# Optimization experiments

Measured on AMD Instinct MI355X. Metric: run time of the kernel, lower is better.

The kernel has to match this reference:

```python
import jax, jax.numpy as jnp
import numpy as np

TEMPERATURE = 0.07
EPS = 1e-20

def setup_inputs() -> dict:
    key = jax.random.key(0)
    k1, k2 = jax.random.split(key)
    B, D, L = 4096, 256, 20
    features = jax.random.normal(k1, (B, D), dtype=jnp.float32)
    labels = jax.random.randint(k2, (B, L), 0, 5)
    return {"features": features, "labels": labels}

def reference(features, labels):
    B = features.shape[0]
    dt = features.dtype
    # [B, B] similarity logits, numerically stabilized (max is detached in torch)
    logits = (features @ features.T) / TEMPERATURE
    logits = logits - jax.lax.stop_gradient(jnp.max(logits, axis=1, keepdims=True))
    logits_mask = 1.0 - jnp.eye(B, dtype=dt)  # exclude self-contrast
    # shared across all label columns (the torch loop recomputes this each iter)
    exp_sum = jnp.sum(jnp.exp(logits) * logits_mask, axis=1, keepdims=True)
    log_prob = logits - jnp.log(exp_sum + EPS)

    def per_label(carry, lab):  # lab: [B] labels for one time-step
        mask = (lab[:, None] == lab[None, :]).astype(dt) * logits_mask  # [B, B]
        pos = mask.sum(1)                                   # positives per anchor
        single = (pos == 0).astype(dt)                      # anchors with no positives
        mean_lp = (mask * log_prob).sum(1) / (pos + single)
        loss_vec = -mean_lp * (1.0 - single)
        loss_i = loss_vec.sum() / (jnp.asarray(B, dt) - single.sum())
        return carry, loss_i

    _, losses = jax.lax.scan(per_label, jnp.float32(0.0), labels.T)  # [L]
    # torch fills minute_loss[:, i] with the scalar loss_i, then takes mean -> mean over i
    return jnp.mean(losses)
```

## Files before the change

### kernel.cpp

```cpp
#include <hip/hip_runtime.h>


#define B_N 4096
#define D_K 256
#define L_N 20
#define INVT 14.285714285714286f

#define CNT_OFF  0x004000u
#define WT_OFF   0x010000u
#define ACC_OFF  0x029000u
#define MP_OFF   0x02A000u
#define EP_OFF   0x02E000u

typedef __bf16 bf16x8 __attribute__((ext_vector_type(8)));
typedef float f32x4 __attribute__((ext_vector_type(4)));

struct __align__(16) U4 { unsigned int x, y, z, w; };

__device__ __forceinline__ U4 pack8(float4 a, float4 b) {
  bf16x8 v;
  v[0] = (__bf16)a.x; v[1] = (__bf16)a.y; v[2] = (__bf16)a.z; v[3] = (__bf16)a.w;
  v[4] = (__bf16)b.x; v[5] = (__bf16)b.y; v[6] = (__bf16)b.z; v[7] = (__bf16)b.w;
  return __builtin_bit_cast(U4, v);
}

__device__ __forceinline__ unsigned int ordf(float x) {
  unsigned int u = __float_as_uint(x);
  return (u & 0x80000000u) ? ~u : (u | 0x80000000u);
}
__device__ __forceinline__ float ordinv(unsigned int o) {
  return __uint_as_float((o & 0x80000000u) ? (o & 0x7FFFFFFFu) : ~o);
}

__global__ __launch_bounds__(512, 2) void k_fused(const float* __restrict__ F,
                                                  const int* __restrict__ lab,
                                                  unsigned char* __restrict__ ws) {
  __shared__ unsigned char smem[67584];
  const int bid = blockIdx.x, t = threadIdx.x;
  if (bid < 256) {
    const int w = t >> 6, l = t & 63;
    const int lr = l & 15, lg = l >> 4;
    const int r = bid & 7, s = bid >> 3;
    const int bm = ((r & 3) << 1) | (s & 1);
    const int bn = ((r >> 2) << 4) | (s >> 1);
    const int rowbase = bm * 512 + w * 64;
    const int colb = bn * 128;
    {
      const int srow = t >> 2, q = t & 3;
      const float* src = F + (colb + srow) * 256 + q * 64;
      #pragma unroll
      for (int i = 0; i < 8; ++i) {
        float4 f0 = *(const float4*)(src + i * 8);
        float4 f1 = *(const float4*)(src + i * 8 + 4);
        const int kb = q * 128 + i * 16;
        *(U4*)(smem + srow * 512 + (kb ^ ((srow & 7) << 4))) = pack8(f0, f1);
      }
    }
    __syncthreads();
    unsigned int* MP = (unsigned int*)(ws + MP_OFF);
    float* EP = (float*)(ws + EP_OFF);
    float* scv = (float*)(smem + 65536);
    const float* arow0 = F + (rowbase + lr) * 256 + lg * 8;
    float ssq[4] = {0.f, 0.f, 0.f, 0.f};
    #pragma unroll 1
    for (int tile = 0; tile < 2; ++tile) {
      f32x4 acc[4][4] = {};
      #pragma unroll 1
      for (int kk = 0; kk < 8; ++kk) {
        bf16x8 afr[4];
        #pragma unroll
        for (int mi = 0; mi < 4; ++mi) {
          const float* ap = arow0 + mi * 16 * 256 + kk * 32;
          float4 a0 = *(const float4*)(ap);
          float4 a1 = *(const float4*)(ap + 4);
          if (tile == 0)
            ssq[mi] += a0.x * a0.x + a0.y * a0.y + a0.z * a0.z + a0.w * a0.w
                     + a1.x * a1.x + a1.y * a1.y + a1.z * a1.z + a1.w * a1.w;
          afr[mi] = __builtin_bit_cast(bf16x8, pack8(a0, a1));
        }
        bf16x8 bfr[4];
        #pragma unroll
        for (int n = 0; n < 4; ++n) {
          const int brow = tile * 64 + n * 16 + lr;
          const int kb = kk * 64 + lg * 16;
          bfr[n] = __builtin_bit_cast(bf16x8,
              *(const U4*)(smem + brow * 512 + (kb ^ ((brow & 7) << 4))));
        }
        #pragma unroll
        for (int mi = 0; mi < 4; ++mi)
          #pragma unroll
          for (int n = 0; n < 4; ++n)
            acc[mi][n] = __builtin_amdgcn_mfma_f32_16x16x32_bf16(afr[mi], bfr[n], acc[mi][n], 0, 0, 0);
      }
      if (tile == 0) {
        #pragma unroll
        for (int mi = 0; mi < 4; ++mi) {
          float ss = ssq[mi];
          ss += __shfl_xor(ss, 16, 64);
          ss += __shfl_xor(ss, 32, 64);
          if (lg == 0) scv[w * 64 + mi * 16 + lr] = ss * INVT;
        }
      }
      #pragma unroll
      for (int mi = 0; mi < 4; ++mi) {
        #pragma unroll
        for (int rr = 0; rr < 4; ++rr) {
          const int row = rowbase + mi * 16 + lg * 4 + rr;
          const float crow = scv[w * 64 + mi * 16 + lg * 4 + rr];
          float vm = -3.4e38f, es = 0.f;
          #pragma unroll
          for (int n = 0; n < 4; ++n) {
            const int col = colb + tile * 64 + n * 16 + lr;
            const float v = acc[mi][n][rr] * INVT;
            vm = fmaxf(vm, v);
            const float e = __expf(v - crow);
            es += (col == row) ? 0.f : e;
          }
          #pragma unroll
          for (int off = 1; off < 16; off <<= 1) {
            vm = fmaxf(vm, __shfl_xor(vm, off, 16));
            es += __shfl_xor(es, off, 16);
          }
          if (lr == 0) {
            atomicMax(MP + row, ordf(vm));
            atomicAdd(EP + row, es);
          }
        }
      }
    }
  } else if (bid < 276) {
    __shared__ int sc[8][5];
    const int l = bid - 256;
    int c0 = 0, c1 = 0, c2 = 0, c3 = 0, c4 = 0;
    for (int j = t; j < B_N; j += 512) {
      int v = lab[j * L_N + l];
      c0 += (v == 0); c1 += (v == 1); c2 += (v == 2); c3 += (v == 3); c4 += (v == 4);
    }
    #pragma unroll
    for (int off = 1; off < 64; off <<= 1) {
      c0 += __shfl_xor(c0, off, 64); c1 += __shfl_xor(c1, off, 64);
      c2 += __shfl_xor(c2, off, 64); c3 += __shfl_xor(c3, off, 64);
      c4 += __shfl_xor(c4, off, 64);
    }
    const int w = t >> 6;
    if ((t & 63) == 0) { sc[w][0] = c0; sc[w][1] = c1; sc[w][2] = c2; sc[w][3] = c3; sc[w][4] = c4; }
    __syncthreads();
    if (t < 5) {
      int s5 = 0;
      #pragma unroll
      for (int ww = 0; ww < 8; ++ww) s5 += sc[ww][t];
      ((int*)(ws + CNT_OFF))[l * 5 + t] = s5;
    }
  } else {
    int* slab = (int*)smem;
    const int idx = bid - 276;
    const int l = idx >> 3, jblk = idx & 7;
    const int j0 = jblk * 512;
    slab[t] = lab[(j0 + t) * L_N + l];
    __syncthreads();
    const int d = t & 255, half = t >> 8;
    const int base = half * 256;
    float a0 = 0, a1 = 0, a2 = 0, a3 = 0, a4 = 0;
    #pragma unroll 16
    for (int jj = 0; jj < 256; ++jj) {
      const int v = slab[base + jj];
      const float x = F[(j0 + base + jj) * 256 + d];
      a0 += (v == 0) ? x : 0.f;
      a1 += (v == 1) ? x : 0.f;
      a2 += (v == 2) ? x : 0.f;
      a3 += (v == 3) ? x : 0.f;
      a4 += (v == 4) ? x : 0.f;
    }
    float* Wt = (float*)(ws + WT_OFF);
    atomicAdd(Wt + (l * 5 + 0) * 256 + d, a0);
    atomicAdd(Wt + (l * 5 + 1) * 256 + d, a1);
    atomicAdd(Wt + (l * 5 + 2) * 256 + d, a2);
    atomicAdd(Wt + (l * 5 + 3) * 256 + d, a3);
    atomicAdd(Wt + (l * 5 + 4) * 256 + d, a4);
  }
}

__global__ __launch_bounds__(1024) void k_final(const float* __restrict__ F,
                                                const int* __restrict__ lab,
                                                unsigned char* __restrict__ ws,
                                                float* __restrict__ out) {
  __shared__ float sL[16][20], sS[16][20];
  const int t = threadIdx.x, w = t >> 6, l = t & 63;
  const int i = blockIdx.x * 16 + w;
  const float4 Ff = *(const float4*)(F + i * 256 + l * 4);
  float ci = Ff.x * Ff.x + Ff.y * Ff.y + Ff.z * Ff.z + Ff.w * Ff.w;
  #pragma unroll
  for (int off = 1; off < 64; off <<= 1) ci += __shfl_xor(ci, off, 64);
  ci *= INVT;
  const float m = ordinv(((const unsigned int*)(ws + MP_OFF))[i]);
  const float e = ((const float*)(ws + EP_OFF))[i];
  const float lp = logf(e * __expf(ci - m) + 1e-20f);
  const float* Wt = (const float*)(ws + WT_OFF);
  const int* cnts = (const int*)(ws + CNT_OFF);
  for (int ll = 0; ll < 20; ++ll) {
    const int v = lab[i * 20 + ll];
    const int cnt = cnts[ll * 5 + v] - 1;
    float lv = 0.f, sg = 0.f;
    if (cnt > 0) {
      const float4 Wf = *(const float4*)(Wt + (ll * 5 + v) * 256 + l * 4);
      float p = Ff.x * Wf.x + Ff.y * Wf.y + Ff.z * Wf.z + Ff.w * Wf.w;
      #pragma unroll
      for (int off = 1; off < 64; off <<= 1) p += __shfl_xor(p, off, 64);
      const float me = p * INVT - ci;
      lv = lp - (me - (float)cnt * m) / (float)cnt;
    } else {
      sg = 1.f;
    }
    if (l == 0) { sL[w][ll] = lv; sS[w][ll] = sg; }
  }
  __syncthreads();
  float* ACC = (float*)(ws + ACC_OFF);
  if (t < 20) {
    float Lsum = 0.f, Ssum = 0.f;
    #pragma unroll
    for (int ww = 0; ww < 16; ++ww) { Lsum += sL[ww][t]; Ssum += sS[ww][t]; }
    atomicAdd(ACC + t, Lsum);
    atomicAdd(ACC + 20 + t, Ssum);
  }
  __syncthreads();
  if (t == 0) {
    __threadfence();
    unsigned int done = atomicAdd((unsigned int*)(ws + ACC_OFF + 160), 1u);
    if (done == 255) {
      float v = 0.f;
      #pragma unroll
      for (int ll = 0; ll < 20; ++ll) {
        float Ls = __hip_atomic_load(ACC + ll, __ATOMIC_RELAXED, __HIP_MEMORY_SCOPE_AGENT);
        float Ss = __hip_atomic_load(ACC + 20 + ll, __ATOMIC_RELAXED, __HIP_MEMORY_SCOPE_AGENT);
        v += Ls / (4096.f - Ss);
      }
      out[0] = v * 0.05f;
    }
  }
}

extern "C" void kernel_launch(void* const* d_in, const int* in_sizes, int n_in,
                              void* d_out, int out_size, void* d_ws, size_t ws_size,
                              hipStream_t stream) {
  const float* F = (const float*)d_in[0];
  const int* lab = (const int*)d_in[1];
  unsigned char* ws = (unsigned char*)d_ws;
  float* out = (float*)d_out;
  hipMemsetAsync(ws + WT_OFF, 0, 0x22000, stream);
  k_fused<<<436, 512, 0, stream>>>(F, lab, ws);
  k_final<<<256, 1024, 0, stream>>>(F, lab, ws, out);
}
```

Measured before the change: 138.7 us.

## Exploit Gram symmetry with triangular tiles and collapse final loss via class-sum norms

The main kernel now computes only the upper-triangular 256x256 tiles of the similarity matrix. Each off-diagonal tile feeds both row-wise and column-wise max and exp-sum updates. Both operand panels are staged in LDS as bf16, and the squared norms are written to a workspace buffer. The final kernel replaces the per-row, per-label dot products with per-class sums, using the identity that the sum of F_i·W_c over a class equals ||W_c||². That removes the second pass over the features. The price is fewer work blocks (136 instead of 256), which may leave compute units idle, plus a larger LDS footprint that limits occupancy.

```diff
diff --git a/kernel.cpp b/kernel.cpp
--- a/kernel.cpp
+++ b/kernel.cpp
@@ -1,9 +1,6 @@
 #include <hip/hip_runtime.h>
 
 
-#define B_N 4096
-#define D_K 256
-#define L_N 20
 #define INVT 14.285714285714286f
 
 #define CNT_OFF  0x004000u
@@ -11,6 +8,7 @@
 #define ACC_OFF  0x029000u
 #define MP_OFF   0x02A000u
 #define EP_OFF   0x02E000u
+#define CV_OFF   0x032000u
 
 typedef __bf16 bf16x8 __attribute__((ext_vector_type(8)));
 typedef float f32x4 __attribute__((ext_vector_type(4)));
@@ -32,108 +30,137 @@
   return __uint_as_float((o & 0x80000000u) ? (o & 0x7FFFFFFFu) : ~o);
 }
 
+__device__ __forceinline__ void stage_panel(const float* __restrict__ F, int gbase, int kh,
+                                            unsigned char* lds, int w, int lr, int lg,
+                                            float& s0, float& s1) {
+  #pragma unroll
+  for (int j = 0; j < 8; ++j) {
+    const int rloc = w * 32 + ((j & 1) << 4) + lr;
+    const int slot = ((j >> 1) << 2) + lg;
+    const float* src = F + (size_t)(gbase + rloc) * 256 + kh * 128 + slot * 8;
+    float4 f0 = *(const float4*)src;
+    float4 f1 = *(const float4*)(src + 4);
+    float ss = f0.x*f0.x + f0.y*f0.y + f0.z*f0.z + f0.w*f0.w
+             + f1.x*f1.x + f1.y*f1.y + f1.z*f1.z + f1.w*f1.w;
+    if (j & 1) s1 += ss; else s0 += ss;
+    *(U4*)(lds + rloc * 256 + ((slot ^ (lr & 7)) << 4)) = pack8(f0, f1);
+  }
+}
+
 __global__ __launch_bounds__(512, 2) void k_fused(const float* __restrict__ F,
                                                   const int* __restrict__ lab,
                                                   unsigned char* __restrict__ ws) {
-  __shared__ unsigned char smem[67584];
+  __shared__ unsigned char smem[133632];
   const int bid = blockIdx.x, t = threadIdx.x;
-  if (bid < 256) {
-    const int w = t >> 6, l = t & 63;
-    const int lr = l & 15, lg = l >> 4;
-    const int r = bid & 7, s = bid >> 3;
-    const int bm = ((r & 3) << 1) | (s & 1);
-    const int bn = ((r >> 2) << 4) | (s >> 1);
-    const int rowbase = bm * 512 + w * 64;
-    const int colb = bn * 128;
-    {
-      const int srow = t >> 2, q = t & 3;
-      const float* src = F + (colb + srow) * 256 + q * 64;
-      #pragma unroll
-      for (int i = 0; i < 8; ++i) {
-        float4 f0 = *(const float4*)(src + i * 8);
-        float4 f1 = *(const float4*)(src + i * 8 + 4);
-        const int kb = q * 128 + i * 16;
-        *(U4*)(smem + srow * 512 + (kb ^ ((srow & 7) << 4))) = pack8(f0, f1);
-      }
-    }
-    __syncthreads();
+  if (bid < 136) {
+    const int w = t >> 6, l = t & 63, lr = l & 15, lg = l >> 4;
+    int I = (int)((sqrtf(8.f * bid + 1.f) - 1.f) * 0.5f);
+    if ((I + 1) * (I + 2) / 2 <= bid) ++I;
+    if (I * (I + 1) / 2 > bid) --I;
+    const int J = bid - I * (I + 1) / 2;
+    const bool diag = (I == J);
+    unsigned char* pA = smem;
+    unsigned char* pB = diag ? smem : smem + 65536;
+    float* scvA = (float*)(smem + 131072);
+    float* scvB = diag ? scvA : scvA + 256;
+    const int wr = w >> 1, wc = w & 1;
+    float sA0 = 0, sA1 = 0, sB0 = 0, sB1 = 0;
+    f32x4 acc[4][8] = {};
+    #pragma unroll 1
+    for (int kh = 0; kh < 2; ++kh) {
+      if (kh) __syncthreads();
+      stage_panel(F, I * 256, kh, pA, w, lr, lg, sA0, sA1);
+      if (!diag) stage_panel(F, J * 256, kh, pB, w, lr, lg, sB0, sB1);
+      __syncthreads();
+      #pragma unroll 1
+      for (int kk = 0; kk < 4; ++kk) {
+        const int sx = ((kk * 4 + lg) ^ (lr & 7)) << 4;
+        bf16x8 afr[4];
+        #pragma unroll
+        for (int mi = 0; mi < 4; ++mi)
+          afr[mi] = *(bf16x8*)(pA + (wr * 64 + mi * 16 + lr) * 256 + sx);
+        #pragma unroll
+        for (int nh = 0; nh < 2; ++nh) {
+          bf16x8 bfr[4];
+          #pragma unroll
+          for (int nn = 0; nn < 4; ++nn)
+            bfr[nn] = *(bf16x8*)(pB + (wc * 128 + (nh * 4 + nn) * 16 + lr) * 256 + sx);
+          #pragma unroll
+          for (int mi = 0; mi < 4; ++mi)
+            #pragma unroll
+            for (int nn = 0; nn < 4; ++nn)
+              acc[mi][nh * 4 + nn] =
+                  __builtin_amdgcn_mfma_f32_16x16x32_bf16(afr[mi], bfr[nn], acc[mi][nh * 4 + nn], 0, 0, 0);
+        }
+      }
+    }
+    sA0 += __shfl_xor(sA0, 16, 64); sA0 += __shfl_xor(sA0, 32, 64);
+    sA1 += __shfl_xor(sA1, 16, 64); sA1 += __shfl_xor(sA1, 32, 64);
+    if (!diag) {
+      sB0 += __shfl_xor(sB0, 16, 64); sB0 += __shfl_xor(sB0, 32, 64);
+      sB1 += __shfl_xor(sB1, 16, 64); sB1 += __shfl_xor(sB1, 32, 64);
+    }
+    if (lg == 0) {
+      scvA[w * 32 + lr] = sA0;
+      scvA[w * 32 + 16 + lr] = sA1;
+      if (!diag) { scvB[w * 32 + lr] = sB0; scvB[w * 32 + 16 + lr] = sB1; }
+    }
+    __syncthreads();
+    if (diag && t < 256) ((float*)(ws + CV_OFF))[I * 256 + t] = scvA[t] * INVT;
     unsigned int* MP = (unsigned int*)(ws + MP_OFF);
     float* EP = (float*)(ws + EP_OFF);
-    float* scv = (float*)(smem + 65536);
-    const float* arow0 = F + (rowbase + lr) * 256 + lg * 8;
-    float ssq[4] = {0.f, 0.f, 0.f, 0.f};
     #pragma unroll 1
-    for (int tile = 0; tile < 2; ++tile) {
-      f32x4 acc[4][4] = {};
+    for (int mi = 0; mi < 4; ++mi) {
+      #pragma unroll
+      for (int r = 0; r < 4; ++r) {
+        const int lrow = wr * 64 + mi * 16 + lg * 4 + r;
+        const int grow = I * 256 + lrow;
+        const float crow = scvA[lrow] * INVT;
+        float vm = -3.4e38f, es = 0.f;
+        #pragma unroll
+        for (int n = 0; n < 8; ++n) {
+          const int gcol = J * 256 + wc * 128 + n * 16 + lr;
+          const float v = acc[mi][n][r] * INVT;
+          vm = fmaxf(vm, v);
+          const float e0 = __expf(v - crow);
+          es += (gcol == grow) ? 0.f : e0;
+        }
+        #pragma unroll
+        for (int off = 1; off < 16; off <<= 1) {
+          vm = fmaxf(vm, __shfl_xor(vm, off, 16));
+          es += __shfl_xor(es, off, 16);
+        }
+        if (lr == 0) { atomicMax(MP + grow, ordf(vm)); atomicAdd(EP + grow, es); }
+      }
+    }
+    if (!diag) {
       #pragma unroll 1
-      for (int kk = 0; kk < 8; ++kk) {
-        bf16x8 afr[4];
-        #pragma unroll
-        for (int mi = 0; mi < 4; ++mi) {
-          const float* ap = arow0 + mi * 16 * 256 + kk * 32;
-          float4 a0 = *(const float4*)(ap);
-          float4 a1 = *(const float4*)(ap + 4);
-          if (tile == 0)
-            ssq[mi] += a0.x * a0.x + a0.y * a0.y + a0.z * a0.z + a0.w * a0.w
-                     + a1.x * a1.x + a1.y * a1.y + a1.z * a1.z + a1.w * a1.w;
-          afr[mi] = __builtin_bit_cast(bf16x8, pack8(a0, a1));
-        }
-        bf16x8 bfr[4];
-        #pragma unroll
-        for (int n = 0; n < 4; ++n) {
-          const int brow = tile * 64 + n * 16 + lr;
-          const int kb = kk * 64 + lg * 16;
-          bfr[n] = __builtin_bit_cast(bf16x8,
-              *(const U4*)(smem + brow * 512 + (kb ^ ((brow & 7) << 4))));
-        }
+      for (int n = 0; n < 8; ++n) {
+        const int lcol = wc * 128 + n * 16 + lr;
+        const int gcol = J * 256 + lcol;
+        const float ccol = scvB[lcol] * INVT;
+        float vm = -3.4e38f, es = 0.f;
         #pragma unroll
         for (int mi = 0; mi < 4; ++mi)
           #pragma unroll
-          for (int n = 0; n < 4; ++n)
-            acc[mi][n] = __builtin_amdgcn_mfma_f32_16x16x32_bf16(afr[mi], bfr[n], acc[mi][n], 0, 0, 0);
-      }
-      if (tile == 0) {
-        #pragma unroll
-        for (int mi = 0; mi < 4; ++mi) {
-          float ss = ssq[mi];
-          ss += __shfl_xor(ss, 16, 64);
-          ss += __shfl_xor(ss, 32, 64);
-          if (lg == 0) scv[w * 64 + mi * 16 + lr] = ss * INVT;
-        }
-      }
-      #pragma unroll
-      for (int mi = 0; mi < 4; ++mi) {
-        #pragma unroll
-        for (int rr = 0; rr < 4; ++rr) {
-          const int row = rowbase + mi * 16 + lg * 4 + rr;
-          const float crow = scv[w * 64 + mi * 16 + lg * 4 + rr];
-          float vm = -3.4e38f, es = 0.f;
-          #pragma unroll
-          for (int n = 0; n < 4; ++n) {
-            const int col = colb + tile * 64 + n * 16 + lr;
-            const float v = acc[mi][n][rr] * INVT;
+          for (int r = 0; r < 4; ++r) {
+            const float v = acc[mi][n][r] * INVT;
             vm = fmaxf(vm, v);
-            const float e = __expf(v - crow);
-            es += (col == row) ? 0.f : e;
+            es += __expf(v - ccol);
           }
-          #pragma unroll
-          for (int off = 1; off < 16; off <<= 1) {
-            vm = fmaxf(vm, __shfl_xor(vm, off, 16));
-            es += __shfl_xor(es, off, 16);
-          }
-          if (lr == 0) {
-            atomicMax(MP + row, ordf(vm));
-            atomicAdd(EP + row, es);
-          }
-        }
-      }
-    }
-  } else if (bid < 276) {
-    __shared__ int sc[8][5];
-    const int l = bid - 256;
+        vm = fmaxf(vm, __shfl_xor(vm, 16, 64));
+        vm = fmaxf(vm, __shfl_xor(vm, 32, 64));
+        es += __shfl_xor(es, 16, 64);
+        es += __shfl_xor(es, 32, 64);
+        if (lg == 0) { atomicMax(MP + gcol, ordf(vm)); atomicAdd(EP + gcol, es); }
+      }
+    }
+  } else if (bid < 156) {
+    int* sc = (int*)smem;
+    const int ll = bid - 136;
     int c0 = 0, c1 = 0, c2 = 0, c3 = 0, c4 = 0;
-    for (int j = t; j < B_N; j += 512) {
-      int v = lab[j * L_N + l];
+    for (int j = t; j < 4096; j += 512) {
+      int v = lab[j * 20 + ll];
       c0 += (v == 0); c1 += (v == 1); c2 += (v == 2); c3 += (v == 3); c4 += (v == 4);
     }
     #pragma unroll
@@ -143,20 +170,20 @@
       c4 += __shfl_xor(c4, off, 64);
     }
     const int w = t >> 6;
-    if ((t & 63) == 0) { sc[w][0] = c0; sc[w][1] = c1; sc[w][2] = c2; sc[w][3] = c3; sc[w][4] = c4; }
+    if ((t & 63) == 0) { sc[w*5+0] = c0; sc[w*5+1] = c1; sc[w*5+2] = c2; sc[w*5+3] = c3; sc[w*5+4] = c4; }
     __syncthreads();
     if (t < 5) {
       int s5 = 0;
       #pragma unroll
-      for (int ww = 0; ww < 8; ++ww) s5 += sc[ww][t];
-      ((int*)(ws + CNT_OFF))[l * 5 + t] = s5;
+      for (int ww = 0; ww < 8; ++ww) s5 += sc[ww*5+t];
+      ((int*)(ws + CNT_OFF))[ll * 5 + t] = s5;
     }
   } else {
     int* slab = (int*)smem;
-    const int idx = bid - 276;
-    const int l = idx >> 3, jblk = idx & 7;
+    const int idx = bid - 156;
+    const int ll = idx >> 3, jblk = idx & 7;
     const int j0 = jblk * 512;
-    slab[t] = lab[(j0 + t) * L_N + l];
+    slab[t] = lab[(j0 + t) * 20 + ll];
     __syncthreads();
     const int d = t & 255, half = t >> 8;
     const int base = half * 256;
@@ -164,7 +191,7 @@
     #pragma unroll 16
     for (int jj = 0; jj < 256; ++jj) {
       const int v = slab[base + jj];
-      const float x = F[(j0 + base + jj) * 256 + d];
+      const float x = F[(size_t)(j0 + base + jj) * 256 + d];
       a0 += (v == 0) ? x : 0.f;
       a1 += (v == 1) ? x : 0.f;
       a2 += (v == 2) ? x : 0.f;
@@ -172,69 +199,77 @@
       a4 += (v == 4) ? x : 0.f;
     }
     float* Wt = (float*)(ws + WT_OFF);
-    atomicAdd(Wt + (l * 5 + 0) * 256 + d, a0);
-    atomicAdd(Wt + (l * 5 + 1) * 256 + d, a1);
-    atomicAdd(Wt + (l * 5 + 2) * 256 + d, a2);
-    atomicAdd(Wt + (l * 5 + 3) * 256 + d, a3);
-    atomicAdd(Wt + (l * 5 + 4) * 256 + d, a4);
-  }
-}
-
-__global__ __launch_bounds__(1024) void k_final(const float* __restrict__ F,
-                                                const int* __restrict__ lab,
-                                                unsigned char* __restrict__ ws,
-                                                float* __restrict__ out) {
-  __shared__ float sL[16][20], sS[16][20];
-  const int t = threadIdx.x, w = t >> 6, l = t & 63;
-  const int i = blockIdx.x * 16 + w;
-  const float4 Ff = *(const float4*)(F + i * 256 + l * 4);
-  float ci = Ff.x * Ff.x + Ff.y * Ff.y + Ff.z * Ff.z + Ff.w * Ff.w;
-  #pragma unroll
-  for (int off = 1; off < 64; off <<= 1) ci += __shfl_xor(ci, off, 64);
-  ci *= INVT;
+    atomicAdd(Wt + (ll * 5 + 0) * 256 + d, a0);
+    atomicAdd(Wt + (ll * 5 + 1) * 256 + d, a1);
+    atomicAdd(Wt + (ll * 5 + 2) * 256 + d, a2);
+    atomicAdd(Wt + (ll * 5 + 3) * 256 + d, a3);
+    atomicAdd(Wt + (ll * 5 + 4) * 256 + d, a4);
+  }
+}
+
+__global__ __launch_bounds__(256) void k_final(const int* __restrict__ lab,
+                                               unsigned char* __restrict__ ws,
+                                               float* __restrict__ out) {
+  __shared__ float sLPM[100], sC[100], wn2[100];
+  __shared__ int isLast;
+  const int t = threadIdx.x;
+  if (t < 100) { sLPM[t] = 0.f; sC[t] = 0.f; }
+  __syncthreads();
+  const int i = blockIdx.x * 256 + t;
   const float m = ordinv(((const unsigned int*)(ws + MP_OFF))[i]);
   const float e = ((const float*)(ws + EP_OFF))[i];
-  const float lp = logf(e * __expf(ci - m) + 1e-20f);
-  const float* Wt = (const float*)(ws + WT_OFF);
-  const int* cnts = (const int*)(ws + CNT_OFF);
+  const float c = ((const float*)(ws + CV_OFF))[i];
+  const float lp = logf(e * __expf(c - m) + 1e-20f);
+  const float val = lp + m;
+  #pragma unroll
   for (int ll = 0; ll < 20; ++ll) {
     const int v = lab[i * 20 + ll];
-    const int cnt = cnts[ll * 5 + v] - 1;
-    float lv = 0.f, sg = 0.f;
-    if (cnt > 0) {
-      const float4 Wf = *(const float4*)(Wt + (ll * 5 + v) * 256 + l * 4);
-      float p = Ff.x * Wf.x + Ff.y * Wf.y + Ff.z * Wf.z + Ff.w * Wf.w;
-      #pragma unroll
-      for (int off = 1; off < 64; off <<= 1) p += __shfl_xor(p, off, 64);
-      const float me = p * INVT - ci;
-      lv = lp - (me - (float)cnt * m) / (float)cnt;
-    } else {
-      sg = 1.f;
-    }
-    if (l == 0) { sL[w][ll] = lv; sS[w][ll] = sg; }
+    atomicAdd(&sLPM[ll * 5 + v], val);
+    atomicAdd(&sC[ll * 5 + v], c);
   }
   __syncthreads();
   float* ACC = (float*)(ws + ACC_OFF);
-  if (t < 20) {
-    float Lsum = 0.f, Ssum = 0.f;
-    #pragma unroll
-    for (int ww = 0; ww < 16; ++ww) { Lsum += sL[ww][t]; Ssum += sS[ww][t]; }
-    atomicAdd(ACC + t, Lsum);
-    atomicAdd(ACC + 20 + t, Ssum);
+  if (t < 100) {
+    atomicAdd(ACC + t, sLPM[t]);
+    atomicAdd(ACC + 100 + t, sC[t]);
   }
   __syncthreads();
   if (t == 0) {
     __threadfence();
-    unsigned int done = atomicAdd((unsigned int*)(ws + ACC_OFF + 160), 1u);
-    if (done == 255) {
-      float v = 0.f;
+    unsigned int done = atomicAdd((unsigned int*)(ws + ACC_OFF + 800), 1u);
+    isLast = (done == 15);
+  }
+  __syncthreads();
+  if (isLast) {
+    const int w = t >> 6, l = t & 63;
+    const float* Wt = (const float*)(ws + WT_OFF);
+    for (int row = w; row < 100; row += 4) {
+      const float4 q = *(const float4*)(Wt + row * 256 + l * 4);
+      float s = q.x * q.x + q.y * q.y + q.z * q.z + q.w * q.w;
       #pragma unroll
+      for (int off = 1; off < 64; off <<= 1) s += __shfl_xor(s, off, 64);
+      if (l == 0) wn2[row] = s;
+    }
+    __syncthreads();
+    if (t == 0) {
+      const int* cnts = (const int*)(ws + CNT_OFF);
+      float loss = 0.f;
       for (int ll = 0; ll < 20; ++ll) {
-        float Ls = __hip_atomic_load(ACC + ll, __ATOMIC_RELAXED, __HIP_MEMORY_SCOPE_AGENT);
-        float Ss = __hip_atomic_load(ACC + 20 + ll, __ATOMIC_RELAXED, __HIP_MEMORY_SCOPE_AGENT);
-        v += Ls / (4096.f - Ss);
-      }
-      out[0] = v * 0.05f;
+        float ls = 0.f, singles = 0.f;
+        for (int v = 0; v < 5; ++v) {
+          const int idx = ll * 5 + v;
+          const int cnt = cnts[idx];
+          if (cnt >= 2) {
+            const float Ls = __hip_atomic_load(ACC + idx, __ATOMIC_RELAXED, __HIP_MEMORY_SCOPE_AGENT);
+            const float Cs = __hip_atomic_load(ACC + 100 + idx, __ATOMIC_RELAXED, __HIP_MEMORY_SCOPE_AGENT);
+            ls += Ls - (wn2[idx] * INVT - Cs) / (float)(cnt - 1);
+          } else if (cnt == 1) {
+            singles += 1.f;
+          }
+        }
+        loss += ls / (4096.f - singles);
+      }
+      out[0] = loss * 0.05f;
     }
   }
 }
@@ -247,6 +282,6 @@
   unsigned char* ws = (unsigned char*)d_ws;
   float* out = (float*)d_out;
   hipMemsetAsync(ws + WT_OFF, 0, 0x22000, stream);
-  k_fused<<<436, 512, 0, stream>>>(F, lab, ws);
-  k_final<<<256, 1024, 0, stream>>>(F, lab, ws, out);
-}
+  k_fused<<<316, 512, 0, stream>>>(F, lab, ws);
+  k_final<<<16, 256, 0, stream>>>(lab, ws, out);
+}
```

New measurement: 199.5 us. 1.44x slower.

## Merge all stages into one persistent kernel with grid barriers and class-sum algebra

Applied to the files above, without the earlier changes.

Replaces the memset plus two kernel launches with a single 256-block kernel. It zeroes the workspace in-kernel and separates the stages with software grid barriers (an atomic counter plus spin-wait). The per-anchor final pass is reformulated so each row's log-sum term and self-similarity are accumulated per (label column, class). The positive-pair dot products are then computed from the squared norms of the per-class feature sums in a single block. This is meant to remove launch and memset overhead and most of the per-anchor dot-product work. In exchange it relies on all blocks being co-resident for the spin barriers, serializes the class-count, class-sum and finalization work behind barriers, and changes the floating-point summation order.

```diff
diff --git a/kernel.cpp b/kernel.cpp
--- a/kernel.cpp
+++ b/kernel.cpp
@@ -1,16 +1,16 @@
 #include <hip/hip_runtime.h>
 
 
-#define B_N 4096
-#define D_K 256
-#define L_N 20
 #define INVT 14.285714285714286f
-
+#define MAGIC 0x5EC7BA11u
+
+#define BAR_OFF  0x000000u
 #define CNT_OFF  0x004000u
 #define WT_OFF   0x010000u
 #define ACC_OFF  0x029000u
 #define MP_OFF   0x02A000u
 #define EP_OFF   0x02E000u
+#define CV_OFF   0x032000u
 
 typedef __bf16 bf16x8 __attribute__((ext_vector_type(8)));
 typedef float f32x4 __attribute__((ext_vector_type(4)));
@@ -32,12 +32,59 @@
   return __uint_as_float((o & 0x80000000u) ? (o & 0x7FFFFFFFu) : ~o);
 }
 
-__global__ __launch_bounds__(512, 2) void k_fused(const float* __restrict__ F,
-                                                  const int* __restrict__ lab,
-                                                  unsigned char* __restrict__ ws) {
+__device__ __forceinline__ void stu(unsigned* p, unsigned v) {
+  __hip_atomic_store(p, v, __ATOMIC_RELAXED, __HIP_MEMORY_SCOPE_AGENT);
+}
+__device__ __forceinline__ void stf(float* p, float v) {
+  __hip_atomic_store(p, v, __ATOMIC_RELAXED, __HIP_MEMORY_SCOPE_AGENT);
+}
+__device__ __forceinline__ float ldf(const float* p) {
+  return __hip_atomic_load(p, __ATOMIC_RELAXED, __HIP_MEMORY_SCOPE_AGENT);
+}
+__device__ __forceinline__ unsigned ldu(const unsigned* p) {
+  return __hip_atomic_load(p, __ATOMIC_RELAXED, __HIP_MEMORY_SCOPE_AGENT);
+}
+__device__ __forceinline__ int ldi(const int* p) {
+  return __hip_atomic_load(p, __ATOMIC_RELAXED, __HIP_MEMORY_SCOPE_AGENT);
+}
+
+__device__ __forceinline__ void gsync(unsigned* ctr, unsigned target) {
+  __syncthreads();
+  if (threadIdx.x == 0) {
+    __threadfence();
+    __hip_atomic_fetch_add(ctr, 1u, __ATOMIC_ACQ_REL, __HIP_MEMORY_SCOPE_AGENT);
+    while (__hip_atomic_load(ctr, __ATOMIC_ACQUIRE, __HIP_MEMORY_SCOPE_AGENT) < target)
+      __builtin_amdgcn_s_sleep(2);
+  }
+  __syncthreads();
+}
+
+__global__ __launch_bounds__(512, 2) void k_mega(const float* __restrict__ F,
+                                                 const int* __restrict__ lab,
+                                                 unsigned char* __restrict__ ws,
+                                                 float* __restrict__ out) {
   __shared__ unsigned char smem[67584];
   const int bid = blockIdx.x, t = threadIdx.x;
-  if (bid < 256) {
+  unsigned* ctr = (unsigned*)(ws + BAR_OFF);
+
+  if (bid == 0 && t == 0) {
+    __hip_atomic_store(ctr, 0u, __ATOMIC_RELAXED, __HIP_MEMORY_SCOPE_AGENT);
+    __hip_atomic_store(ctr + 1, MAGIC, __ATOMIC_RELEASE, __HIP_MEMORY_SCOPE_AGENT);
+  }
+  if (t == 0) {
+    while (__hip_atomic_load(ctr + 1, __ATOMIC_ACQUIRE, __HIP_MEMORY_SCOPE_AGENT) != MAGIC)
+      __builtin_amdgcn_s_sleep(2);
+  }
+  __syncthreads();
+
+  {
+    unsigned* z = (unsigned*)(ws + WT_OFF);
+    const int n = 0x22000 / 4;
+    for (int k = bid * 512 + t; k < n; k += 256 * 512) stu(z + k, 0u);
+  }
+  gsync(ctr, 256);
+
+  {
     const int w = t >> 6, l = t & 63;
     const int lr = l & 15, lg = l >> 4;
     const int r = bid & 7, s = bid >> 3;
@@ -47,7 +94,7 @@
     const int colb = bn * 128;
     {
       const int srow = t >> 2, q = t & 3;
-      const float* src = F + (colb + srow) * 256 + q * 64;
+      const float* src = F + (size_t)(colb + srow) * 256 + q * 64;
       #pragma unroll
       for (int i = 0; i < 8; ++i) {
         float4 f0 = *(const float4*)(src + i * 8);
@@ -59,8 +106,9 @@
     __syncthreads();
     unsigned int* MP = (unsigned int*)(ws + MP_OFF);
     float* EP = (float*)(ws + EP_OFF);
+    float* CV = (float*)(ws + CV_OFF);
     float* scv = (float*)(smem + 65536);
-    const float* arow0 = F + (rowbase + lr) * 256 + lg * 8;
+    const float* arow0 = F + (size_t)(rowbase + lr) * 256 + lg * 8;
     float ssq[4] = {0.f, 0.f, 0.f, 0.f};
     #pragma unroll 1
     for (int tile = 0; tile < 2; ++tile) {
@@ -98,7 +146,11 @@
           float ss = ssq[mi];
           ss += __shfl_xor(ss, 16, 64);
           ss += __shfl_xor(ss, 32, 64);
-          if (lg == 0) scv[w * 64 + mi * 16 + lr] = ss * INVT;
+          if (lg == 0) {
+            const float ci = ss * INVT;
+            scv[w * 64 + mi * 16 + lr] = ci;
+            if (colb == 0) stf(CV + rowbase + mi * 16 + lr, ci);
+          }
         }
       }
       #pragma unroll
@@ -113,8 +165,8 @@
             const int col = colb + tile * 64 + n * 16 + lr;
             const float v = acc[mi][n][rr] * INVT;
             vm = fmaxf(vm, v);
-            const float e = __expf(v - crow);
-            es += (col == row) ? 0.f : e;
+            const float e0 = __expf(v - crow);
+            es += (col == row) ? 0.f : e0;
           }
           #pragma unroll
           for (int off = 1; off < 16; off <<= 1) {
@@ -128,35 +180,14 @@
         }
       }
     }
-  } else if (bid < 276) {
-    __shared__ int sc[8][5];
-    const int l = bid - 256;
-    int c0 = 0, c1 = 0, c2 = 0, c3 = 0, c4 = 0;
-    for (int j = t; j < B_N; j += 512) {
-      int v = lab[j * L_N + l];
-      c0 += (v == 0); c1 += (v == 1); c2 += (v == 2); c3 += (v == 3); c4 += (v == 4);
-    }
-    #pragma unroll
-    for (int off = 1; off < 64; off <<= 1) {
-      c0 += __shfl_xor(c0, off, 64); c1 += __shfl_xor(c1, off, 64);
-      c2 += __shfl_xor(c2, off, 64); c3 += __shfl_xor(c3, off, 64);
-      c4 += __shfl_xor(c4, off, 64);
-    }
-    const int w = t >> 6;
-    if ((t & 63) == 0) { sc[w][0] = c0; sc[w][1] = c1; sc[w][2] = c2; sc[w][3] = c3; sc[w][4] = c4; }
-    __syncthreads();
-    if (t < 5) {
-      int s5 = 0;
-      #pragma unroll
-      for (int ww = 0; ww < 8; ++ww) s5 += sc[ww][t];
-      ((int*)(ws + CNT_OFF))[l * 5 + t] = s5;
-    }
-  } else {
+  }
+
+  __syncthreads();
+  if (bid < 160) {
     int* slab = (int*)smem;
-    const int idx = bid - 276;
-    const int l = idx >> 3, jblk = idx & 7;
+    const int ll = bid >> 3, jblk = bid & 7;
     const int j0 = jblk * 512;
-    slab[t] = lab[(j0 + t) * L_N + l];
+    slab[t] = lab[(j0 + t) * 20 + ll];
     __syncthreads();
     const int d = t & 255, half = t >> 8;
     const int base = half * 256;
@@ -164,7 +195,7 @@
     #pragma unroll 16
     for (int jj = 0; jj < 256; ++jj) {
       const int v = slab[base + jj];
-      const float x = F[(j0 + base + jj) * 256 + d];
+      const float x = F[(size_t)(j0 + base + jj) * 256 + d];
       a0 += (v == 0) ? x : 0.f;
       a1 += (v == 1) ? x : 0.f;
       a2 += (v == 2) ? x : 0.f;
@@ -172,69 +203,97 @@
       a4 += (v == 4) ? x : 0.f;
     }
     float* Wt = (float*)(ws + WT_OFF);
-    atomicAdd(Wt + (l * 5 + 0) * 256 + d, a0);
-    atomicAdd(Wt + (l * 5 + 1) * 256 + d, a1);
-    atomicAdd(Wt + (l * 5 + 2) * 256 + d, a2);
-    atomicAdd(Wt + (l * 5 + 3) * 256 + d, a3);
-    atomicAdd(Wt + (l * 5 + 4) * 256 + d, a4);
-  }
-}
-
-__global__ __launch_bounds__(1024) void k_final(const float* __restrict__ F,
-                                                const int* __restrict__ lab,
-                                                unsigned char* __restrict__ ws,
-                                                float* __restrict__ out) {
-  __shared__ float sL[16][20], sS[16][20];
-  const int t = threadIdx.x, w = t >> 6, l = t & 63;
-  const int i = blockIdx.x * 16 + w;
-  const float4 Ff = *(const float4*)(F + i * 256 + l * 4);
-  float ci = Ff.x * Ff.x + Ff.y * Ff.y + Ff.z * Ff.z + Ff.w * Ff.w;
-  #pragma unroll
-  for (int off = 1; off < 64; off <<= 1) ci += __shfl_xor(ci, off, 64);
-  ci *= INVT;
-  const float m = ordinv(((const unsigned int*)(ws + MP_OFF))[i]);
-  const float e = ((const float*)(ws + EP_OFF))[i];
-  const float lp = logf(e * __expf(ci - m) + 1e-20f);
-  const float* Wt = (const float*)(ws + WT_OFF);
-  const int* cnts = (const int*)(ws + CNT_OFF);
-  for (int ll = 0; ll < 20; ++ll) {
-    const int v = lab[i * 20 + ll];
-    const int cnt = cnts[ll * 5 + v] - 1;
-    float lv = 0.f, sg = 0.f;
-    if (cnt > 0) {
-      const float4 Wf = *(const float4*)(Wt + (ll * 5 + v) * 256 + l * 4);
-      float p = Ff.x * Wf.x + Ff.y * Wf.y + Ff.z * Wf.z + Ff.w * Wf.w;
-      #pragma unroll
-      for (int off = 1; off < 64; off <<= 1) p += __shfl_xor(p, off, 64);
-      const float me = p * INVT - ci;
-      lv = lp - (me - (float)cnt * m) / (float)cnt;
-    } else {
-      sg = 1.f;
-    }
-    if (l == 0) { sL[w][ll] = lv; sS[w][ll] = sg; }
-  }
-  __syncthreads();
-  float* ACC = (float*)(ws + ACC_OFF);
-  if (t < 20) {
-    float Lsum = 0.f, Ssum = 0.f;
+    atomicAdd(Wt + (ll * 5 + 0) * 256 + d, a0);
+    atomicAdd(Wt + (ll * 5 + 1) * 256 + d, a1);
+    atomicAdd(Wt + (ll * 5 + 2) * 256 + d, a2);
+    atomicAdd(Wt + (ll * 5 + 3) * 256 + d, a3);
+    atomicAdd(Wt + (ll * 5 + 4) * 256 + d, a4);
+  } else if (bid < 180) {
+    int* sc = (int*)smem;
+    const int ll = bid - 160;
+    int c0 = 0, c1 = 0, c2 = 0, c3 = 0, c4 = 0;
+    for (int j = t; j < 4096; j += 512) {
+      int v = lab[j * 20 + ll];
+      c0 += (v == 0); c1 += (v == 1); c2 += (v == 2); c3 += (v == 3); c4 += (v == 4);
+    }
     #pragma unroll
-    for (int ww = 0; ww < 16; ++ww) { Lsum += sL[ww][t]; Ssum += sS[ww][t]; }
-    atomicAdd(ACC + t, Lsum);
-    atomicAdd(ACC + 20 + t, Ssum);
-  }
-  __syncthreads();
-  if (t == 0) {
-    __threadfence();
-    unsigned int done = atomicAdd((unsigned int*)(ws + ACC_OFF + 160), 1u);
-    if (done == 255) {
-      float v = 0.f;
+    for (int off = 1; off < 64; off <<= 1) {
+      c0 += __shfl_xor(c0, off, 64); c1 += __shfl_xor(c1, off, 64);
+      c2 += __shfl_xor(c2, off, 64); c3 += __shfl_xor(c3, off, 64);
+      c4 += __shfl_xor(c4, off, 64);
+    }
+    const int w = t >> 6;
+    if ((t & 63) == 0) { sc[w*5+0] = c0; sc[w*5+1] = c1; sc[w*5+2] = c2; sc[w*5+3] = c3; sc[w*5+4] = c4; }
+    __syncthreads();
+    if (t < 5) {
+      int s5 = 0;
+      #pragma unroll
+      for (int ww = 0; ww < 8; ++ww) s5 += sc[ww * 5 + t];
+      stu((unsigned*)(ws + CNT_OFF) + ll * 5 + t, (unsigned)s5);
+    }
+  }
+  gsync(ctr, 512);
+
+  {
+    float* sLPM = (float*)smem;
+    float* sC = (float*)smem + 128;
+    if (t < 100) { sLPM[t] = 0.f; sC[t] = 0.f; }
+    __syncthreads();
+    if (t < 16) {
+      const int i = bid * 16 + t;
+      const float m = ordinv(ldu((const unsigned*)(ws + MP_OFF) + i));
+      const float e = ldf((const float*)(ws + EP_OFF) + i);
+      const float c = ldf((const float*)(ws + CV_OFF) + i);
+      const float val = logf(e * __expf(c - m) + 1e-20f) + m;
       #pragma unroll
       for (int ll = 0; ll < 20; ++ll) {
-        float Ls = __hip_atomic_load(ACC + ll, __ATOMIC_RELAXED, __HIP_MEMORY_SCOPE_AGENT);
-        float Ss = __hip_atomic_load(ACC + 20 + ll, __ATOMIC_RELAXED, __HIP_MEMORY_SCOPE_AGENT);
-        v += Ls / (4096.f - Ss);
-      }
-      out[0] = v * 0.05f;
+        const int v = lab[i * 20 + ll];
+        atomicAdd(&sLPM[ll * 5 + v], val);
+        atomicAdd(&sC[ll * 5 + v], c);
+      }
+    }
+    __syncthreads();
+    float* ACC = (float*)(ws + ACC_OFF);
+    if (t < 100) {
+      atomicAdd(ACC + t, sLPM[t]);
+      atomicAdd(ACC + 100 + t, sC[t]);
+    }
+  }
+  gsync(ctr, 768);
+
+  if (bid == 0) {
+    float* wn2 = (float*)(smem + 1024);
+    const int w = t >> 6, l = t & 63;
+    const float* Wt = (const float*)(ws + WT_OFF);
+    for (int row = w; row < 100; row += 8) {
+      const float* p = Wt + row * 256 + l * 4;
+      float q0 = ldf(p), q1 = ldf(p + 1), q2 = ldf(p + 2), q3 = ldf(p + 3);
+      float s = q0 * q0 + q1 * q1 + q2 * q2 + q3 * q3;
+      #pragma unroll
+      for (int off = 1; off < 64; off <<= 1) s += __shfl_xor(s, off, 64);
+      if (l == 0) wn2[row] = s;
+    }
+    __syncthreads();
+    if (t == 0) {
+      const float* ACC = (const float*)(ws + ACC_OFF);
+      const int* cnts = (const int*)(ws + CNT_OFF);
+      float loss = 0.f;
+      for (int ll = 0; ll < 20; ++ll) {
+        float ls = 0.f, singles = 0.f;
+        for (int v = 0; v < 5; ++v) {
+          const int idx = ll * 5 + v;
+          const int cnt = ldi(cnts + idx);
+          if (cnt >= 2) {
+            const float Ls = ldf(ACC + idx);
+            const float Cs = ldf(ACC + 100 + idx);
+            ls += Ls - (wn2[idx] * INVT - Cs) / (float)(cnt - 1);
+          } else if (cnt == 1) {
+            singles += 1.f;
+          }
+        }
+        loss += ls / (4096.f - singles);
+      }
+      out[0] = loss * 0.05f;
     }
   }
 }
@@ -246,7 +305,5 @@
   const int* lab = (const int*)d_in[1];
   unsigned char* ws = (unsigned char*)d_ws;
   float* out = (float*)d_out;
-  hipMemsetAsync(ws + WT_OFF, 0, 0x22000, stream);
-  k_fused<<<436, 512, 0, stream>>>(F, lab, ws);
-  k_final<<<256, 1024, 0, stream>>>(F, lab, ws, out);
-}
+  k_mega<<<256, 512, 0, stream>>>(F, lab, ws, out);
+}
```

Result: slower. 365.0 us (+163.1%).
